# Performance work log

Hardware: AMD Instinct MI355X
Metric: run time of the kernel (lower is better)

The kernel has to match this reference:

```python
import jax, jax.numpy as jnp
import numpy as np

B, S, D, H = 4, 1024, 1024, 16
HD = D // H  # 64, even for RoPE


def _rope_tables(seq_len, head_dim):
    inv_freq = 1.0 / (10000.0 ** (jnp.arange(0, head_dim, 2, dtype=jnp.float32) / head_dim))
    pos = jnp.arange(seq_len, dtype=jnp.float32)
    ang = pos[:, None] * inv_freq[None, :]           # [S, HD/2]
    return jnp.cos(ang), jnp.sin(ang)


def _apply_rope(x, cos, sin):
    # x: [B, S, H, HD]; cos/sin: [S, HD/2] broadcast to [1, S, 1, HD/2]
    c = cos[None, :, None, :]
    s = sin[None, :, None, :]
    x1 = x[..., 0::2]
    x2 = x[..., 1::2]
    return jnp.concatenate([x1 * c - x2 * s, x1 * s + x2 * c], axis=-1)


def setup_inputs() -> dict:
    key = jax.random.key(0)
    ks = jax.random.split(key, 11)
    sc = 1.0 / np.sqrt(D)
    inp = {
        "query": jax.random.normal(ks[0], (B, S, D), jnp.float32),
        "key": jax.random.normal(ks[1], (B, S, D), jnp.float32),
        "value": jax.random.normal(ks[2], (B, S, D), jnp.float32),
        "mask": jnp.tril(jnp.ones((S, S), jnp.int32))[None, None],  # causal [1,1,S,S]
        "Wq": jax.random.normal(ks[3], (D, D), jnp.float32) * sc,
        "bq": jnp.zeros((D,), jnp.float32),
        "Wk": jax.random.normal(ks[4], (D, D), jnp.float32) * sc,
        "bk": jnp.zeros((D,), jnp.float32),
        "Wv": jax.random.normal(ks[5], (D, D), jnp.float32) * sc,
        "bv": jnp.zeros((D,), jnp.float32),
        "Wo": jax.random.normal(ks[6], (D, D), jnp.float32) * sc,
        "bo": jnp.zeros((D,), jnp.float32),
    }
    return inp


def reference(query, key, value, mask, Wq, bq, Wk, bk, Wv, bv, Wo, bo):
    Bq, Sq, _ = query.shape
    Sk = key.shape[1]
    q = (query @ Wq + bq).reshape(Bq, Sq, H, HD)
    k = (key @ Wk + bk).reshape(Bq, Sk, H, HD)
    v = (value @ Wv + bv).reshape(Bq, Sk, H, HD)
    cos, sin = _rope_tables(max(Sq, Sk), HD)
    q = _apply_rope(q, cos[:Sq], sin[:Sq])
    k = _apply_rope(k, cos[:Sk], sin[:Sk])
    scores = jnp.einsum("bqhd,bkhd->bhqk", q, k) / jnp.sqrt(jnp.float32(HD))
    scores = jnp.where(mask == 0, jnp.float32(-jnp.inf), scores)
    attn = jax.nn.softmax(scores, axis=-1)  # dropout p=0 (inference)
    ctx = jnp.einsum("bhqk,bkhd->bqhd", attn, v).reshape(Bq, Sq, D)
    return ctx @ Wo + bo
```

## Files before the change

### kernel.cpp

```cpp
#include <hip/hip_runtime.h>
#include <hip/hip_bf16.h>
#include <math.h>

#define B_DIM 4
#define S_DIM 1024
#define D_DIM 1024
#define H_DIM 16
#define HD_DIM 64
#define M_TOT 4096

typedef short short8 __attribute__((ext_vector_type(8)));
typedef float f32x4 __attribute__((ext_vector_type(4)));

__device__ inline float bf2f(short u)
{
    return __uint_as_float(((unsigned)(unsigned short)u) << 16);
}

__device__ inline void gload_lds16(const void* gsrc, void* lds)
{
    __builtin_amdgcn_global_load_lds(
        (const __attribute__((address_space(1))) unsigned int*)gsrc,
        (__attribute__((address_space(3))) unsigned int*)lds, 16, 0, 0);
}

__global__ __launch_bounds__(256) void rope_table_kernel(float* __restrict__ tab)
{
    const int t = blockIdx.x * 256 + threadIdx.x;
    const int pos = t >> 5, i = t & 31;
    float inv = powf(10000.0f, -(float)(2 * i) / 64.0f);
    float ang = (float)pos * inv;
    float s, c;
    sincosf(ang, &s, &c);
    tab[t] = c;
    tab[32768 + t] = s;
}

__global__ __launch_bounds__(256) void convert3_kernel(
    const float* __restrict__ S0, const float* __restrict__ S1,
    const float* __restrict__ S2,
    __hip_bfloat16* __restrict__ D0, __hip_bfloat16* __restrict__ D1,
    __hip_bfloat16* __restrict__ D2)
{
    const float* src = (blockIdx.y == 0) ? S0 : (blockIdx.y == 1) ? S1 : S2;
    __hip_bfloat16* dst = (blockIdx.y == 0) ? D0 : (blockIdx.y == 1) ? D1 : D2;
    const int base = (blockIdx.x * 256 + threadIdx.x) * 4;
    float4 v = *(const float4*)(src + base);
    __hip_bfloat16 o[4];
    o[0] = __float2bfloat16(v.x);
    o[1] = __float2bfloat16(v.y);
    o[2] = __float2bfloat16(v.z);
    o[3] = __float2bfloat16(v.w);
    *(uint2*)(dst + base) = *(uint2*)o;
}

__global__ __launch_bounds__(256) void transpose4_to_bf16_kernel(
    const float* __restrict__ W0, const float* __restrict__ W1,
    const float* __restrict__ W2, const float* __restrict__ W3,
    __hip_bfloat16* __restrict__ T0, __hip_bfloat16* __restrict__ T1,
    __hip_bfloat16* __restrict__ T2, __hip_bfloat16* __restrict__ T3)
{
    const float* W = (blockIdx.z == 0) ? W0 : (blockIdx.z == 1) ? W1
                    : (blockIdx.z == 2) ? W2 : W3;
    __hip_bfloat16* T = (blockIdx.z == 0) ? T0 : (blockIdx.z == 1) ? T1
                       : (blockIdx.z == 2) ? T2 : T3;

    __shared__ float tile[32][33];
    const int tid = threadIdx.x;
    const int r = tid >> 3;
    const int c4 = (tid & 7) * 4;

    float4 v = *(const float4*)&W[(long)(blockIdx.y * 32 + r) * D_DIM + blockIdx.x * 32 + c4];
    tile[r][c4 + 0] = v.x;
    tile[r][c4 + 1] = v.y;
    tile[r][c4 + 2] = v.z;
    tile[r][c4 + 3] = v.w;
    __syncthreads();

    __hip_bfloat16 o[4];
    o[0] = __float2bfloat16(tile[c4 + 0][r]);
    o[1] = __float2bfloat16(tile[c4 + 1][r]);
    o[2] = __float2bfloat16(tile[c4 + 2][r]);
    o[3] = __float2bfloat16(tile[c4 + 3][r]);
    *(uint2*)&T[(long)(blockIdx.x * 32 + r) * D_DIM + blockIdx.y * 32 + c4] = *(uint2*)o;
}

__global__ __launch_bounds__(256, 3) void gemm_qkv_kernel(
    const __hip_bfloat16* __restrict__ Xq, const __hip_bfloat16* __restrict__ Xk,
    const __hip_bfloat16* __restrict__ Xv,
    const __hip_bfloat16* __restrict__ WtQ, const __hip_bfloat16* __restrict__ WtK,
    const __hip_bfloat16* __restrict__ WtV,
    const float* __restrict__ bq, const float* __restrict__ bk,
    const float* __restrict__ bv,
    __hip_bfloat16* __restrict__ Qo, __hip_bfloat16* __restrict__ Ko,
    __hip_bfloat16* __restrict__ Vto,
    const float* __restrict__ tab)
{
    __shared__ __align__(16) __hip_bfloat16 Al[128][32];
    __shared__ __align__(16) __hip_bfloat16 Bl[128][32];

    const int F = blockIdx.x + 8 * blockIdx.y + 256 * blockIdx.z;
    const int xcd = F & 7;
    const int s = F >> 3;
    const int z = s >> 5;
    const int n0 = (s & 7) * 128;
    const int m0 = ((xcd << 2) | ((s >> 3) & 3)) * 128;

    const __hip_bfloat16* X = (z == 0) ? Xq : (z == 1) ? Xk : Xv;
    const __hip_bfloat16* Wt = (z == 0) ? WtQ : (z == 1) ? WtK : WtV;
    const float* bias = (z == 0) ? bq : (z == 1) ? bk : bv;

    const int tid = threadIdx.x;
    const int l = tid & 63;
    const int w = tid >> 6;

    const int srow = w * 16 + (l >> 2);
    const int skc = (l & 3) * 8;
    const __hip_bfloat16* Abase = X + (long)(m0 + srow) * D_DIM + skc;
    const __hip_bfloat16* Bbase = Wt + (long)(n0 + srow) * D_DIM + skc;
    char* ldsA0 = (char*)&Al[0][0] + w * 1024;
    char* ldsB0 = (char*)&Bl[0][0] + w * 1024;

    const int lrow = l & 15;
    const int kg = l >> 4;
    const int wr = (w >> 1) * 64;
    const int wc = (w & 1) * 64;

    f32x4 acc[4][4];
#pragma unroll
    for (int i = 0; i < 4; ++i)
#pragma unroll
        for (int j = 0; j < 4; ++j) acc[i][j] = (f32x4){0.f, 0.f, 0.f, 0.f};

    for (int k0 = 0; k0 < D_DIM; k0 += 32) {
        __syncthreads();
        gload_lds16(Abase + k0, ldsA0);
        gload_lds16(Abase + 64 * D_DIM + k0, ldsA0 + 4096);
        gload_lds16(Bbase + k0, ldsB0);
        gload_lds16(Bbase + 64 * D_DIM + k0, ldsB0 + 4096);
        __syncthreads();

        short8 af[4], bf[4];
#pragma unroll
        for (int i = 0; i < 4; ++i)
            af[i] = *(const short8*)&Al[wr + i * 16 + lrow][kg * 8];
#pragma unroll
        for (int j = 0; j < 4; ++j)
            bf[j] = *(const short8*)&Bl[wc + j * 16 + lrow][kg * 8];
#pragma unroll
        for (int i = 0; i < 4; ++i)
#pragma unroll
            for (int j = 0; j < 4; ++j)
                acc[i][j] = __builtin_amdgcn_mfma_f32_16x16x32_bf16(
                    af[i], bf[j], acc[i][j], 0, 0, 0);
    }

    if (z < 2) {
        __hip_bfloat16* Out = (z == 0) ? Qo : Ko;
        const float scale = (z == 0) ? 0.125f : 1.0f;
#pragma unroll
        for (int i = 0; i < 4; ++i) {
#pragma unroll
            for (int j = 0; j < 4; ++j) {
                const int col = n0 + wc + j * 16 + lrow;
                const float bvs = bias[col];
                const int odd = col & 1;
                const int ip = (col & 63) >> 1;
                const int ocol = (col & ~63) + ip + (odd ? 32 : 0);
                const int rbase = m0 + wr + i * 16 + kg * 4;
#pragma unroll
                for (int r = 0; r < 4; ++r) {
                    const int row = rbase + r;
                    const int pos = row & (S_DIM - 1);
                    float x = acc[i][j][r] + bvs;
                    float xo = __shfl_xor(x, 1);
                    float x1 = odd ? xo : x;
                    float x2 = odd ? x : xo;
                    float cv = tab[pos * 32 + ip];
                    float sv = tab[32768 + pos * 32 + ip];
                    float res = odd ? (x1 * sv + x2 * cv) : (x1 * cv - x2 * sv);
                    Out[(long)row * D_DIM + ocol] = __float2bfloat16(res * scale);
                }
            }
        }
    } else {
#pragma unroll
        for (int i = 0; i < 4; ++i) {
#pragma unroll
            for (int j = 0; j < 4; ++j) {
                const int col = n0 + wc + j * 16 + lrow;
                const float bvs = bias[col];
                const int hh = col >> 6, dd = col & 63;
                const int rbase = m0 + wr + i * 16 + kg * 4;
                const int bb = rbase >> 10, s0 = rbase & 1023;
                __hip_bfloat16 o[4];
#pragma unroll
                for (int r = 0; r < 4; ++r)
                    o[r] = __float2bfloat16(acc[i][j][r] + bvs);
                *(uint2*)&Vto[((long)((bb * H_DIM + hh) * HD_DIM + dd)) * S_DIM + s0] =
                    *(uint2*)o;
            }
        }
    }
}

__global__ __launch_bounds__(256, 2) void gemm_wo_kernel(
    const __hip_bfloat16* __restrict__ X, const __hip_bfloat16* __restrict__ Wt,
    const float* __restrict__ bias, float* __restrict__ Out)
{
    __shared__ __align__(16) __hip_bfloat16 Al[128][32];
    __shared__ __align__(16) __hip_bfloat16 Bl[64][32];

    const int F = blockIdx.x;
    const int xcd = F & 7;
    const int s = F >> 3;
    const int n0 = (s & 15) * 64;
    const int m0 = ((xcd << 2) | (s >> 4)) * 128;

    const int tid = threadIdx.x;
    const int l = tid & 63;
    const int w = tid >> 6;

    const int srow = w * 16 + (l >> 2);
    const int skc = (l & 3) * 8;
    const __hip_bfloat16* Abase = X + (long)(m0 + srow) * D_DIM + skc;
    const __hip_bfloat16* Bbase = Wt + (long)(n0 + srow) * D_DIM + skc;
    char* ldsA0 = (char*)&Al[0][0] + w * 1024;
    char* ldsB0 = (char*)&Bl[0][0] + w * 1024;

    const int lrow = l & 15;
    const int kg = l >> 4;
    const int wr = (w >> 1) * 64;
    const int wc = (w & 1) * 32;

    f32x4 acc[4][2];
#pragma unroll
    for (int i = 0; i < 4; ++i)
#pragma unroll
        for (int j = 0; j < 2; ++j) acc[i][j] = (f32x4){0.f, 0.f, 0.f, 0.f};

    for (int k0 = 0; k0 < D_DIM; k0 += 32) {
        __syncthreads();
        gload_lds16(Abase + k0, ldsA0);
        gload_lds16(Abase + 64 * D_DIM + k0, ldsA0 + 4096);
        gload_lds16(Bbase + k0, ldsB0);
        __syncthreads();

        short8 af[4], bf[2];
#pragma unroll
        for (int i = 0; i < 4; ++i)
            af[i] = *(const short8*)&Al[wr + i * 16 + lrow][kg * 8];
#pragma unroll
        for (int j = 0; j < 2; ++j)
            bf[j] = *(const short8*)&Bl[wc + j * 16 + lrow][kg * 8];
#pragma unroll
        for (int i = 0; i < 4; ++i)
#pragma unroll
            for (int j = 0; j < 2; ++j)
                acc[i][j] = __builtin_amdgcn_mfma_f32_16x16x32_bf16(
                    af[i], bf[j], acc[i][j], 0, 0, 0);
    }

#pragma unroll
    for (int i = 0; i < 4; ++i) {
#pragma unroll
        for (int j = 0; j < 2; ++j) {
            const int col = n0 + wc + j * 16 + lrow;
            const float bv = bias[col];
            const int rbase = m0 + wr + i * 16 + kg * 4;
#pragma unroll
            for (int r = 0; r < 4; ++r)
                Out[(long)(rbase + r) * D_DIM + col] = acc[i][j][r] + bv;
        }
    }
}

#define KPAD 72

__global__ __launch_bounds__(256, 2) void attn_mfma_kernel(
    const __hip_bfloat16* __restrict__ Q,
    const __hip_bfloat16* __restrict__ K,
    const __hip_bfloat16* __restrict__ Vt,
    __hip_bfloat16* __restrict__ CTX)
{
    __shared__ __align__(16) __hip_bfloat16 Kl[64][KPAD];
    __shared__ __align__(16) __hip_bfloat16 Vl[64][KPAD];
    __shared__ __align__(16) __hip_bfloat16 Pl[4][32][KPAD];
    __shared__ __align__(16) float aS[4][2][16];

    const int tid = threadIdx.x;
    const int l = tid & 63;
    const int w = tid >> 6;

    const int bid = blockIdx.x + 8 * blockIdx.y + 128 * blockIdx.z;
    const int half = bid >> 8;
    const int idx = bid & 255;
    int qt = idx & 7;
    if (half) qt = 7 - qt;
    const int rest = idx >> 3;
    const int h = rest & 15;
    const int b = (rest >> 4) | (half << 1);

    const int lrow = l & 15;
    const int kg = l >> 4;
    const int kg4 = kg * 4;

    const int q0w = qt * 128 + w * 32;
    const long qrow_base = (long)b * S_DIM + q0w;

    short8 qf[2][2];
#pragma unroll
    for (int m = 0; m < 2; ++m)
#pragma unroll
        for (int ks = 0; ks < 2; ++ks)
            qf[m][ks] = *(const short8*)&Q[(qrow_base + m * 16 + lrow) * D_DIM +
                                           h * HD_DIM + ks * 32 + kg * 8];

    f32x4 ctx[2][4];
#pragma unroll
    for (int m = 0; m < 2; ++m)
#pragma unroll
        for (int d = 0; d < 4; ++d) ctx[m][d] = (f32x4){0.f, 0.f, 0.f, 0.f};
    float mrun[2] = {-1e30f, -1e30f};
    float lrun[2] = {0.f, 0.f};

    const int sr = tid >> 2;
    const int sc2 = (tid & 3) * 16;
    const __hip_bfloat16* Kg = K + ((long)b * S_DIM + sr) * D_DIM + h * HD_DIM + sc2;
    const __hip_bfloat16* Vg = Vt + ((long)((b * H_DIM + h) * HD_DIM) + sr) * S_DIM + sc2;

    const int ktmax = 2 * qt + 1;

    short8 kp0 = *(const short8*)Kg;
    short8 kp1 = *(const short8*)(Kg + 8);
    short8 vp0 = *(const short8*)Vg;
    short8 vp1 = *(const short8*)(Vg + 8);

    for (int kt = 0; kt <= ktmax; ++kt) {
        __syncthreads();
        *(short8*)&Kl[sr][sc2]     = kp0;
        *(short8*)&Kl[sr][sc2 + 8] = kp1;
        *(short8*)&Vl[sr][sc2]     = vp0;
        *(short8*)&Vl[sr][sc2 + 8] = vp1;
        if (kt < ktmax) {
            const __hip_bfloat16* kp = Kg + (long)(kt + 1) * 64 * D_DIM;
            const __hip_bfloat16* vp = Vg + (kt + 1) * 64;
            kp0 = *(const short8*)kp;
            kp1 = *(const short8*)(kp + 8);
            vp0 = *(const short8*)vp;
            vp1 = *(const short8*)(vp + 8);
        }
        __syncthreads();

        if (kt * 64 > q0w + 31) continue;

        f32x4 sac[2][4];
#pragma unroll
        for (int m = 0; m < 2; ++m)
#pragma unroll
            for (int nt = 0; nt < 4; ++nt) sac[m][nt] = (f32x4){0.f, 0.f, 0.f, 0.f};

        short8 kf[4][2];
#pragma unroll
        for (int nt = 0; nt < 4; ++nt)
#pragma unroll
            for (int ks = 0; ks < 2; ++ks)
                kf[nt][ks] = *(const short8*)&Kl[nt * 16 + lrow][ks * 32 + kg * 8];
#pragma unroll
        for (int m = 0; m < 2; ++m)
#pragma unroll
            for (int nt = 0; nt < 4; ++nt)
#pragma unroll
                for (int ks = 0; ks < 2; ++ks)
                    sac[m][nt] = __builtin_amdgcn_mfma_f32_16x16x32_bf16(
                        kf[nt][ks], qf[m][ks], sac[m][nt], 0, 0, 0);

        const bool partial = (kt * 64 + 63 > q0w);
        const int kbase = kt * 64;
#pragma unroll
        for (int m = 0; m < 2; ++m) {
            const int qg = q0w + m * 16 + lrow;
            float s[16];
#pragma unroll
            for (int nt = 0; nt < 4; ++nt)
#pragma unroll
                for (int r = 0; r < 4; ++r) {
                    float v = sac[m][nt][r];
                    if (partial && (kbase + nt * 16 + kg4 + r > qg)) v = -1e30f;
                    s[nt * 4 + r] = v;
                }
            float t8[8];
#pragma unroll
            for (int i = 0; i < 8; ++i) t8[i] = fmaxf(s[i], s[i + 8]);
#pragma unroll
            for (int i = 0; i < 4; ++i) t8[i] = fmaxf(t8[i], t8[i + 4]);
            float mx = fmaxf(fmaxf(t8[0], t8[1]), fmaxf(t8[2], t8[3]));
            mx = fmaxf(mx, __shfl_xor(mx, 16));
            mx = fmaxf(mx, __shfl_xor(mx, 32));
            const float mnew = fmaxf(mrun[m], mx);
            const float alpha = __expf(mrun[m] - mnew);
            mrun[m] = mnew;

            float p0s = 0.f, p1s = 0.f, p2s = 0.f, p3s = 0.f;
            __attribute__((aligned(8))) __hip_bfloat16 pb[16];
#pragma unroll
            for (int i = 0; i < 4; ++i) {
                float p = __expf(s[i] - mnew);      p0s += p; pb[i] = __float2bfloat16(p);
            }
#pragma unroll
            for (int i = 4; i < 8; ++i) {
                float p = __expf(s[i] - mnew);      p1s += p; pb[i] = __float2bfloat16(p);
            }
#pragma unroll
            for (int i = 8; i < 12; ++i) {
                float p = __expf(s[i] - mnew);      p2s += p; pb[i] = __float2bfloat16(p);
            }
#pragma unroll
            for (int i = 12; i < 16; ++i) {
                float p = __expf(s[i] - mnew);      p3s += p; pb[i] = __float2bfloat16(p);
            }
            float sum = (p0s + p1s) + (p2s + p3s);
            sum += __shfl_xor(sum, 16);
            sum += __shfl_xor(sum, 32);
            lrun[m] = lrun[m] * alpha + sum;

            if (kg == 0) aS[w][m][lrow] = alpha;
#pragma unroll
            for (int nt = 0; nt < 4; ++nt)
                *(uint2*)&Pl[w][m * 16 + lrow][nt * 16 + kg4] = *(uint2*)&pb[nt * 4];
        }

#pragma unroll
        for (int m = 0; m < 2; ++m) {
            f32x4 al4 = *(const f32x4*)&aS[w][m][kg4];
#pragma unroll
            for (int dt = 0; dt < 4; ++dt)
#pragma unroll
                for (int r = 0; r < 4; ++r) ctx[m][dt][r] *= al4[r];
        }

        short8 vf[4][2];
#pragma unroll
        for (int dt = 0; dt < 4; ++dt)
#pragma unroll
            for (int ks = 0; ks < 2; ++ks)
                vf[dt][ks] = *(const short8*)&Vl[dt * 16 + lrow][ks * 32 + kg * 8];
#pragma unroll
        for (int m = 0; m < 2; ++m) {
            short8 pf[2];
#pragma unroll
            for (int ks = 0; ks < 2; ++ks)
                pf[ks] = *(const short8*)&Pl[w][m * 16 + lrow][ks * 32 + kg * 8];
#pragma unroll
            for (int dt = 0; dt < 4; ++dt)
#pragma unroll
                for (int ks = 0; ks < 2; ++ks)
                    ctx[m][dt] = __builtin_amdgcn_mfma_f32_16x16x32_bf16(
                        pf[ks], vf[dt][ks], ctx[m][dt], 0, 0, 0);
        }
    }

    if (kg == 0) {
        aS[w][0][lrow] = lrun[0];
        aS[w][1][lrow] = lrun[1];
    }
#pragma unroll
    for (int m = 0; m < 2; ++m) {
        f32x4 lv = *(const f32x4*)&aS[w][m][kg4];
#pragma unroll
        for (int r = 0; r < 4; ++r) {
            const float inv_l = 1.0f / lv[r];
            const long rowoff = (qrow_base + m * 16 + kg4 + r) * D_DIM + h * HD_DIM;
#pragma unroll
            for (int dt = 0; dt < 4; ++dt)
                CTX[rowoff + dt * 16 + lrow] = __float2bfloat16(ctx[m][dt][r] * inv_l);
        }
    }
}

extern "C" void kernel_launch(void* const* d_in, const int* in_sizes, int n_in,
                              void* d_out, int out_size, void* d_ws, size_t ws_size,
                              hipStream_t stream)
{
    const float* query = (const float*)d_in[0];
    const float* key   = (const float*)d_in[1];
    const float* value = (const float*)d_in[2];
    const float* Wq = (const float*)d_in[4];
    const float* bq = (const float*)d_in[5];
    const float* Wk = (const float*)d_in[6];
    const float* bk = (const float*)d_in[7];
    const float* Wv = (const float*)d_in[8];
    const float* bv = (const float*)d_in[9];
    const float* Wo = (const float*)d_in[10];
    const float* bo = (const float*)d_in[11];

    char* wsb = (char*)d_ws;
    __hip_bfloat16* Xqb   = (__hip_bfloat16*)(wsb);
    __hip_bfloat16* Xkb   = (__hip_bfloat16*)(wsb + (8L  << 20));
    __hip_bfloat16* Xvb   = (__hip_bfloat16*)(wsb + (16L << 20));
    __hip_bfloat16* Qr    = (__hip_bfloat16*)(wsb + (24L << 20));
    __hip_bfloat16* Kr    = (__hip_bfloat16*)(wsb + (32L << 20));
    __hip_bfloat16* Vtb   = (__hip_bfloat16*)(wsb + (40L << 20));
    __hip_bfloat16* CTXbf = (__hip_bfloat16*)(wsb + (48L << 20));
    __hip_bfloat16* WtQ   = (__hip_bfloat16*)(wsb + (56L << 20));
    __hip_bfloat16* WtK   = (__hip_bfloat16*)(wsb + (58L << 20));
    __hip_bfloat16* WtV   = (__hip_bfloat16*)(wsb + (60L << 20));
    __hip_bfloat16* WtO   = (__hip_bfloat16*)(wsb + (62L << 20));
    float*          tab   = (float*)(wsb + (64L << 20));

    rope_table_kernel<<<128, 256, 0, stream>>>(tab);
    transpose4_to_bf16_kernel<<<dim3(32, 32, 4), 256, 0, stream>>>(
        Wq, Wk, Wv, Wo, WtQ, WtK, WtV, WtO);
    convert3_kernel<<<dim3(4096, 3), 256, 0, stream>>>(
        query, key, value, Xqb, Xkb, Xvb);

    gemm_qkv_kernel<<<dim3(8, 32, 3), 256, 0, stream>>>(
        Xqb, Xkb, Xvb, WtQ, WtK, WtV, bq, bk, bv, Qr, Kr, Vtb, tab);

    attn_mfma_kernel<<<dim3(8, 16, 4), 256, 0, stream>>>(Qr, Kr, Vtb, CTXbf);

    gemm_wo_kernel<<<512, 256, 0, stream>>>(CTXbf, WtO, bo, (float*)d_out);
}
```

Baseline: 126.3 us.

## Fuse input bf16 conversion into QKV GEMM and double-buffer both GEMMs' LDS

Drops the separate fp32→bf16 conversion kernel. The QKV GEMM now loads fp32 activations directly, converts them in registers and writes them to a padded LDS tile, which removes a full read/write pass over the three inputs. Both the QKV and output-projection GEMMs switch to double-buffered LDS, prefetching the next K slice while MFMAs run on the current one, and use an XOR swizzle on the K offset to cut LDS bank conflicts. The trade-offs are more LDS per block, which can lower occupancy, and twice the global bytes per A load, since fp32 tiles are re-read for each N tile.

```diff
diff --git a/kernel.cpp b/kernel.cpp
--- a/kernel.cpp
+++ b/kernel.cpp
@@ -36,24 +36,6 @@
     tab[32768 + t] = s;
 }
 
-__global__ __launch_bounds__(256) void convert3_kernel(
-    const float* __restrict__ S0, const float* __restrict__ S1,
-    const float* __restrict__ S2,
-    __hip_bfloat16* __restrict__ D0, __hip_bfloat16* __restrict__ D1,
-    __hip_bfloat16* __restrict__ D2)
-{
-    const float* src = (blockIdx.y == 0) ? S0 : (blockIdx.y == 1) ? S1 : S2;
-    __hip_bfloat16* dst = (blockIdx.y == 0) ? D0 : (blockIdx.y == 1) ? D1 : D2;
-    const int base = (blockIdx.x * 256 + threadIdx.x) * 4;
-    float4 v = *(const float4*)(src + base);
-    __hip_bfloat16 o[4];
-    o[0] = __float2bfloat16(v.x);
-    o[1] = __float2bfloat16(v.y);
-    o[2] = __float2bfloat16(v.z);
-    o[3] = __float2bfloat16(v.w);
-    *(uint2*)(dst + base) = *(uint2*)o;
-}
-
 __global__ __launch_bounds__(256) void transpose4_to_bf16_kernel(
     const float* __restrict__ W0, const float* __restrict__ W1,
     const float* __restrict__ W2, const float* __restrict__ W3,
@@ -86,8 +68,8 @@
 }
 
 __global__ __launch_bounds__(256, 3) void gemm_qkv_kernel(
-    const __hip_bfloat16* __restrict__ Xq, const __hip_bfloat16* __restrict__ Xk,
-    const __hip_bfloat16* __restrict__ Xv,
+    const float* __restrict__ Xq, const float* __restrict__ Xk,
+    const float* __restrict__ Xv,
     const __hip_bfloat16* __restrict__ WtQ, const __hip_bfloat16* __restrict__ WtK,
     const __hip_bfloat16* __restrict__ WtV,
     const float* __restrict__ bq, const float* __restrict__ bk,
@@ -96,17 +78,17 @@
     __hip_bfloat16* __restrict__ Vto,
     const float* __restrict__ tab)
 {
-    __shared__ __align__(16) __hip_bfloat16 Al[128][32];
-    __shared__ __align__(16) __hip_bfloat16 Bl[128][32];
+    __shared__ __align__(16) __hip_bfloat16 Al[2][128][40];
+    __shared__ __align__(16) __hip_bfloat16 Bl[2][128][32];
 
     const int F = blockIdx.x + 8 * blockIdx.y + 256 * blockIdx.z;
     const int xcd = F & 7;
-    const int s = F >> 3;
-    const int z = s >> 5;
-    const int n0 = (s & 7) * 128;
-    const int m0 = ((xcd << 2) | ((s >> 3) & 3)) * 128;
-
-    const __hip_bfloat16* X = (z == 0) ? Xq : (z == 1) ? Xk : Xv;
+    const int sb = F >> 3;
+    const int z = sb >> 5;
+    const int n0 = (sb & 7) * 128;
+    const int m0 = ((xcd << 2) | ((sb >> 3) & 3)) * 128;
+
+    const float* X = (z == 0) ? Xq : (z == 1) ? Xk : Xv;
     const __hip_bfloat16* Wt = (z == 0) ? WtQ : (z == 1) ? WtK : WtV;
     const float* bias = (z == 0) ? bq : (z == 1) ? bk : bv;
 
@@ -115,14 +97,16 @@
     const int w = tid >> 6;
 
     const int srow = w * 16 + (l >> 2);
-    const int skc = (l & 3) * 8;
-    const __hip_bfloat16* Abase = X + (long)(m0 + srow) * D_DIM + skc;
-    const __hip_bfloat16* Bbase = Wt + (long)(n0 + srow) * D_DIM + skc;
-    char* ldsA0 = (char*)&Al[0][0] + w * 1024;
-    char* ldsB0 = (char*)&Bl[0][0] + w * 1024;
+    const int sk = ((l & 3) ^ ((l >> 2) & 3)) * 8;
+    const __hip_bfloat16* Bbase = Wt + (long)(n0 + srow) * D_DIM + sk;
+
+    const int arow = tid >> 1;
+    const int ak = (tid & 1) * 16;
+    const float* Af = X + (long)(m0 + arow) * D_DIM + ak;
 
     const int lrow = l & 15;
     const int kg = l >> 4;
+    const int ksw = (kg ^ (lrow & 3)) * 8;
     const int wr = (w >> 1) * 64;
     const int wc = (w & 1) * 64;
 
@@ -132,27 +116,66 @@
 #pragma unroll
         for (int j = 0; j < 4; ++j) acc[i][j] = (f32x4){0.f, 0.f, 0.f, 0.f};
 
-    for (int k0 = 0; k0 < D_DIM; k0 += 32) {
-        __syncthreads();
-        gload_lds16(Abase + k0, ldsA0);
-        gload_lds16(Abase + 64 * D_DIM + k0, ldsA0 + 4096);
-        gload_lds16(Bbase + k0, ldsB0);
-        gload_lds16(Bbase + 64 * D_DIM + k0, ldsB0 + 4096);
-        __syncthreads();
+    {
+        char* ldsB = (char*)&Bl[0][0][0] + w * 1024;
+        gload_lds16(Bbase, ldsB);
+        gload_lds16(Bbase + 64 * D_DIM, ldsB + 4096);
+        float4 f0 = *(const float4*)(Af);
+        float4 f1 = *(const float4*)(Af + 4);
+        float4 f2 = *(const float4*)(Af + 8);
+        float4 f3 = *(const float4*)(Af + 12);
+        float fa[16] = {f0.x, f0.y, f0.z, f0.w, f1.x, f1.y, f1.z, f1.w,
+                        f2.x, f2.y, f2.z, f2.w, f3.x, f3.y, f3.z, f3.w};
+        __attribute__((aligned(16))) __hip_bfloat16 ab[16];
+#pragma unroll
+        for (int i = 0; i < 16; ++i) ab[i] = __float2bfloat16(fa[i]);
+        *(short8*)&Al[0][arow][ak]     = ((const short8*)ab)[0];
+        *(short8*)&Al[0][arow][ak + 8] = ((const short8*)ab)[1];
+    }
+    __syncthreads();
+
+#pragma unroll 2
+    for (int t = 0; t < 32; ++t) {
+        const int cur = t & 1;
+        const int nxt = cur ^ 1;
+        const bool more = (t < 31);
+
+        float4 f0, f1, f2, f3;
+        if (more) {
+            const int k0n = (t + 1) * 32;
+            char* ldsB = (char*)&Bl[nxt][0][0] + w * 1024;
+            gload_lds16(Bbase + k0n, ldsB);
+            gload_lds16(Bbase + 64 * D_DIM + k0n, ldsB + 4096);
+            f0 = *(const float4*)(Af + k0n);
+            f1 = *(const float4*)(Af + k0n + 4);
+            f2 = *(const float4*)(Af + k0n + 8);
+            f3 = *(const float4*)(Af + k0n + 12);
+        }
 
         short8 af[4], bf[4];
 #pragma unroll
         for (int i = 0; i < 4; ++i)
-            af[i] = *(const short8*)&Al[wr + i * 16 + lrow][kg * 8];
+            af[i] = *(const short8*)&Al[cur][wr + i * 16 + lrow][kg * 8];
 #pragma unroll
         for (int j = 0; j < 4; ++j)
-            bf[j] = *(const short8*)&Bl[wc + j * 16 + lrow][kg * 8];
+            bf[j] = *(const short8*)&Bl[cur][wc + j * 16 + lrow][ksw];
 #pragma unroll
         for (int i = 0; i < 4; ++i)
 #pragma unroll
             for (int j = 0; j < 4; ++j)
                 acc[i][j] = __builtin_amdgcn_mfma_f32_16x16x32_bf16(
                     af[i], bf[j], acc[i][j], 0, 0, 0);
+
+        if (more) {
+            float fa[16] = {f0.x, f0.y, f0.z, f0.w, f1.x, f1.y, f1.z, f1.w,
+                            f2.x, f2.y, f2.z, f2.w, f3.x, f3.y, f3.z, f3.w};
+            __attribute__((aligned(16))) __hip_bfloat16 ab[16];
+#pragma unroll
+            for (int i = 0; i < 16; ++i) ab[i] = __float2bfloat16(fa[i]);
+            *(short8*)&Al[nxt][arow][ak]     = ((const short8*)ab)[0];
+            *(short8*)&Al[nxt][arow][ak + 8] = ((const short8*)ab)[1];
+        }
+        __syncthreads();
     }
 
     if (z < 2) {
@@ -208,8 +231,8 @@
     const __hip_bfloat16* __restrict__ X, const __hip_bfloat16* __restrict__ Wt,
     const float* __restrict__ bias, float* __restrict__ Out)
 {
-    __shared__ __align__(16) __hip_bfloat16 Al[128][32];
-    __shared__ __align__(16) __hip_bfloat16 Bl[64][32];
+    __shared__ __align__(16) __hip_bfloat16 Al[2][128][32];
+    __shared__ __align__(16) __hip_bfloat16 Bl[2][64][32];
 
     const int F = blockIdx.x;
     const int xcd = F & 7;
@@ -222,14 +245,13 @@
     const int w = tid >> 6;
 
     const int srow = w * 16 + (l >> 2);
-    const int skc = (l & 3) * 8;
-    const __hip_bfloat16* Abase = X + (long)(m0 + srow) * D_DIM + skc;
-    const __hip_bfloat16* Bbase = Wt + (long)(n0 + srow) * D_DIM + skc;
-    char* ldsA0 = (char*)&Al[0][0] + w * 1024;
-    char* ldsB0 = (char*)&Bl[0][0] + w * 1024;
+    const int sk = ((l & 3) ^ ((l >> 2) & 3)) * 8;
+    const __hip_bfloat16* Abase = X + (long)(m0 + srow) * D_DIM + sk;
+    const __hip_bfloat16* Bbase = Wt + (long)(n0 + srow) * D_DIM + sk;
 
     const int lrow = l & 15;
     const int kg = l >> 4;
+    const int ksw = (kg ^ (lrow & 3)) * 8;
     const int wr = (w >> 1) * 64;
     const int wc = (w & 1) * 32;
 
@@ -239,26 +261,42 @@
 #pragma unroll
         for (int j = 0; j < 2; ++j) acc[i][j] = (f32x4){0.f, 0.f, 0.f, 0.f};
 
-    for (int k0 = 0; k0 < D_DIM; k0 += 32) {
-        __syncthreads();
-        gload_lds16(Abase + k0, ldsA0);
-        gload_lds16(Abase + 64 * D_DIM + k0, ldsA0 + 4096);
-        gload_lds16(Bbase + k0, ldsB0);
-        __syncthreads();
+    {
+        char* ldsA = (char*)&Al[0][0][0] + w * 1024;
+        char* ldsB = (char*)&Bl[0][0][0] + w * 1024;
+        gload_lds16(Abase, ldsA);
+        gload_lds16(Abase + 64 * D_DIM, ldsA + 4096);
+        gload_lds16(Bbase, ldsB);
+    }
+    __syncthreads();
+
+#pragma unroll 2
+    for (int t = 0; t < 32; ++t) {
+        const int cur = t & 1;
+        const int nxt = cur ^ 1;
+        if (t < 31) {
+            const int k0n = (t + 1) * 32;
+            char* ldsA = (char*)&Al[nxt][0][0] + w * 1024;
+            char* ldsB = (char*)&Bl[nxt][0][0] + w * 1024;
+            gload_lds16(Abase + k0n, ldsA);
+            gload_lds16(Abase + 64 * D_DIM + k0n, ldsA + 4096);
+            gload_lds16(Bbase + k0n, ldsB);
+        }
 
         short8 af[4], bf[2];
 #pragma unroll
         for (int i = 0; i < 4; ++i)
-            af[i] = *(const short8*)&Al[wr + i * 16 + lrow][kg * 8];
+            af[i] = *(const short8*)&Al[cur][wr + i * 16 + lrow][ksw];
 #pragma unroll
         for (int j = 0; j < 2; ++j)
-            bf[j] = *(const short8*)&Bl[wc + j * 16 + lrow][kg * 8];
+            bf[j] = *(const short8*)&Bl[cur][wc + j * 16 + lrow][ksw];
 #pragma unroll
         for (int i = 0; i < 4; ++i)
 #pragma unroll
             for (int j = 0; j < 2; ++j)
                 acc[i][j] = __builtin_amdgcn_mfma_f32_16x16x32_bf16(
                     af[i], bf[j], acc[i][j], 0, 0, 0);
+        __syncthreads();
     }
 
 #pragma unroll
@@ -495,27 +533,22 @@
     const float* bo = (const float*)d_in[11];
 
     char* wsb = (char*)d_ws;
-    __hip_bfloat16* Xqb   = (__hip_bfloat16*)(wsb);
-    __hip_bfloat16* Xkb   = (__hip_bfloat16*)(wsb + (8L  << 20));
-    __hip_bfloat16* Xvb   = (__hip_bfloat16*)(wsb + (16L << 20));
-    __hip_bfloat16* Qr    = (__hip_bfloat16*)(wsb + (24L << 20));
-    __hip_bfloat16* Kr    = (__hip_bfloat16*)(wsb + (32L << 20));
-    __hip_bfloat16* Vtb   = (__hip_bfloat16*)(wsb + (40L << 20));
-    __hip_bfloat16* CTXbf = (__hip_bfloat16*)(wsb + (48L << 20));
-    __hip_bfloat16* WtQ   = (__hip_bfloat16*)(wsb + (56L << 20));
-    __hip_bfloat16* WtK   = (__hip_bfloat16*)(wsb + (58L << 20));
-    __hip_bfloat16* WtV   = (__hip_bfloat16*)(wsb + (60L << 20));
-    __hip_bfloat16* WtO   = (__hip_bfloat16*)(wsb + (62L << 20));
-    float*          tab   = (float*)(wsb + (64L << 20));
+    __hip_bfloat16* Qr    = (__hip_bfloat16*)(wsb);
+    __hip_bfloat16* Kr    = (__hip_bfloat16*)(wsb + (8L  << 20));
+    __hip_bfloat16* Vtb   = (__hip_bfloat16*)(wsb + (16L << 20));
+    __hip_bfloat16* CTXbf = (__hip_bfloat16*)(wsb + (24L << 20));
+    __hip_bfloat16* WtQ   = (__hip_bfloat16*)(wsb + (32L << 20));
+    __hip_bfloat16* WtK   = (__hip_bfloat16*)(wsb + (34L << 20));
+    __hip_bfloat16* WtV   = (__hip_bfloat16*)(wsb + (36L << 20));
+    __hip_bfloat16* WtO   = (__hip_bfloat16*)(wsb + (38L << 20));
+    float*          tab   = (float*)(wsb + (40L << 20));
 
     rope_table_kernel<<<128, 256, 0, stream>>>(tab);
     transpose4_to_bf16_kernel<<<dim3(32, 32, 4), 256, 0, stream>>>(
         Wq, Wk, Wv, Wo, WtQ, WtK, WtV, WtO);
-    convert3_kernel<<<dim3(4096, 3), 256, 0, stream>>>(
-        query, key, value, Xqb, Xkb, Xvb);
 
     gemm_qkv_kernel<<<dim3(8, 32, 3), 256, 0, stream>>>(
-        Xqb, Xkb, Xvb, WtQ, WtK, WtV, bq, bk, bv, Qr, Kr, Vtb, tab);
+        query, key, value, WtQ, WtK, WtV, bq, bk, bv, Qr, Kr, Vtb, tab);
 
     attn_mfma_kernel<<<dim3(8, 16, 4), 256, 0, stream>>>(Qr, Kr, Vtb, CTXbf);
 
```

New measurement: 132.9 us. +5.2%, slower.
